# Performance work log

Measured on AMD Instinct MI355X. Metric: run time of the kernel, lower is better.

The kernel has to match this reference:

```python
import jax, jax.numpy as jnp
import numpy as np

B, N, E, D, H, O = 4, 10000, 160000, 128, 4, 64
NEG_SLOPE = 0.2  # PyG GATConv default


def setup_inputs() -> dict:
    key = jax.random.key(0)
    ks = jax.random.split(key, 9)
    x = jax.random.normal(ks[0], (B, N, D), jnp.float32)
    edge_index = jax.random.randint(ks[1], (2, E), 0, N, dtype=jnp.int64)
    edge_attr = jax.random.uniform(ks[2], (E,), jnp.float32)
    W_src = jax.random.normal(ks[3], (D, H, O), jnp.float32) * (1.0 / np.sqrt(D))
    att_src = jax.random.normal(ks[4], (H, O), jnp.float32) * 0.1
    att_dst = jax.random.normal(ks[5], (H, O), jnp.float32) * 0.1
    W_edge = jax.random.normal(ks[6], (H, O), jnp.float32) * 0.1  # lin_edge weight for edge_dim=1
    att_edge = jax.random.normal(ks[7], (H, O), jnp.float32) * 0.1
    bias = jnp.zeros((O,), jnp.float32)
    return {"x": x, "edge_index": edge_index, "edge_attr": edge_attr,
            "W_src": W_src, "att_src": att_src, "att_dst": att_dst,
            "W_edge": W_edge, "att_edge": att_edge, "bias": bias}


def reference(x, edge_index, edge_attr, W_src, att_src, att_dst, W_edge, att_edge, bias):
    src, dst = edge_index[0], edge_index[1]
    # shared linear projection (PyG non-bipartite GATConv): [B,N,H,O]
    h = jnp.einsum('bnd,dho->bnho', x, W_src)
    a_src = jnp.einsum('bnho,ho->bnh', h, att_src)  # [B,N,H]
    a_dst = jnp.einsum('bnho,ho->bnh', h, att_dst)  # [B,N,H]
    # edge feature projection (edge_dim=1): [E,H]
    a_edge = edge_attr[:, None] * jnp.einsum('ho,ho->h', W_edge, att_edge)[None, :]
    # attention logits per edge: [B,E,H]
    alpha = a_src[:, src] + a_dst[:, dst] + a_edge[None]
    alpha = jax.nn.leaky_relu(alpha, NEG_SLOPE)
    # segment softmax over destination nodes; segment ops need axis 0 = E
    alpha_t = jnp.transpose(alpha, (1, 0, 2))  # [E,B,H]
    m = jax.ops.segment_max(alpha_t, dst, num_segments=N)  # [N,B,H]
    m = jnp.where(jnp.isfinite(m), m, 0.0)
    p = jnp.exp(alpha_t - m[dst])
    s = jax.ops.segment_sum(p, dst, num_segments=N)
    w = p / jnp.maximum(s[dst], jnp.asarray(1e-16, p.dtype))  # [E,B,H]
    # weighted messages from source nodes, scatter-add into destinations
    msg = w[..., None] * jnp.transpose(h[:, src], (1, 0, 2, 3))  # [E,B,H,O]
    out = jax.ops.segment_sum(msg, dst, num_segments=N)  # [N,B,H,O]
    out = out.mean(axis=2) + bias  # concat=False -> mean over heads, [N,B,O]
    return jnp.transpose(out, (1, 0, 2))  # [B,N,O]
```

## Files before the change

### kernel.cpp

```cpp
#include <hip/hip_runtime.h>
#include <hip/hip_fp16.h>
#include <math.h>

constexpr int B_  = 4;
constexpr int N_  = 10000;
constexpr int E_  = 160000;
constexpr int D_  = 128;
constexpr int H_  = 4;
constexpr int O_  = 64;
constexpr float NEG_SLOPE = 0.2f;
constexpr int CAP = 64;
constexpr int PLACE_BLOCKS = E_ / 256;
constexpr int GEMM_BLOCKS  = (B_ * N_) / 64;

using half8   = __attribute__((ext_vector_type(8))) _Float16;
using half2v  = __attribute__((ext_vector_type(2))) _Float16;
using f32x4   = __attribute__((ext_vector_type(4))) float;
using ushort8v = __attribute__((ext_vector_type(8))) unsigned short;

static __device__ __forceinline__ unsigned short f2h(float f) {
    return __half_as_ushort(__float2half(f));
}
static __device__ __forceinline__ float h2f(unsigned short u) {
    return __half2float(__ushort_as_half(u));
}

#if __has_builtin(__builtin_amdgcn_fdot2)
#define FDOT2(a, b, c) __builtin_amdgcn_fdot2((a), (b), (c), false)
#else
static __device__ __forceinline__ float FDOT2(half2v a, half2v b, float c) {
    return c + (float)a[0] * (float)b[0] + (float)a[1] * (float)b[1];
}
#endif

__global__ __launch_bounds__(256) void k_prep(
    const float* __restrict__ Wsrc, const float* __restrict__ att_src,
    const float* __restrict__ att_dst,
    const float* __restrict__ W_edge, const float* __restrict__ att_edge,
    unsigned short* __restrict__ W1t, unsigned short* __restrict__ Vt,
    int* __restrict__ deg, float* __restrict__ c)
{
    const int d = blockIdx.x;
    const int t = threadIdx.x;
    const int h = t >> 6;

    for (int i = d * 256 + t; i < N_; i += 128 * 256) deg[i] = 0;

    const float wv = Wsrc[(size_t)d * 256 + t];
    const int cc = ((t & 63) << 2) | h;
    W1t[(size_t)cc * 128 + d] = f2h(wv);

    float vs = wv * att_src[t];
    float vd = wv * att_dst[t];
#pragma unroll
    for (int off = 32; off > 0; off >>= 1) {
        vs += __shfl_down(vs, off, 64);
        vd += __shfl_down(vd, off, 64);
    }
    if ((t & 63) == 0) {
        Vt[h * 128 + d]       = f2h(vs);
        Vt[(4 + h) * 128 + d] = f2h(vd);
    }
    if (d == 1) {
#pragma unroll
        for (int k = 0; k < 4; ++k) Vt[1024 + k * 256 + t] = 0;
    }

    if (d == 0) {
        float v = W_edge[t] * att_edge[t];
#pragma unroll
        for (int off = 32; off > 0; off >>= 1) v += __shfl_down(v, off, 64);
        if ((t & 63) == 0) c[h] = v;
    }
}

__global__ __launch_bounds__(256) void k_gemm(
    const float* __restrict__ x, const int* __restrict__ ei,
    const float* __restrict__ eattr,
    const unsigned short* __restrict__ W1t, const unsigned short* __restrict__ Vt,
    unsigned short* __restrict__ hbw, float* __restrict__ asrc, float* __restrict__ adst,
    int* __restrict__ deg, int2* __restrict__ srcea)
{
    constexpr int APAD = 136;
    __shared__ uint4 SHq[2112];
    unsigned short* A0 = (unsigned short*)SHq;
    unsigned short* A1 = (unsigned short*)SHq + 4352;
    unsigned short* Cb = (unsigned short*)SHq + 8704;

    const int t = threadIdx.x;

    if (blockIdx.x < PLACE_BLOCKS) {
        const int e = blockIdx.x * 256 + t;
        const int dstn = ei[E_ + e];
        const int r = atomicAdd(&deg[dstn], 1);
        srcea[dstn * CAP + r] = make_int2(ei[e], __float_as_int(eattr[e]));
        return;
    }

    const int w = t >> 6;
    const int lane = t & 63;
    const int i = lane & 15;
    const int q = lane >> 4;
    const size_t rowbase = (size_t)(blockIdx.x - PLACE_BLOCKS) * 64;

    const float4* xg = (const float4*)(x + rowbase * D_);
    float4 xr0[4], xr1[4];
#pragma unroll
    for (int it = 0; it < 4; ++it) xr0[it] = xg[it * 256 + t];
#pragma unroll
    for (int it = 0; it < 4; ++it) xr1[it] = xg[1024 + it * 256 + t];

    half8 breg[4][4];
#pragma unroll
    for (int ks = 0; ks < 4; ++ks)
#pragma unroll
        for (int ctl = 0; ctl < 4; ++ctl) {
            const size_t boff = (size_t)((w * 4 + ctl) * 16 + i) * 128 + ks * 32 + q * 8;
            breg[ks][ctl] = *(const half8*)&W1t[boff];
        }
    half8 vreg[4];
    if (w < 2) {
#pragma unroll
        for (int ks = 0; ks < 4; ++ks)
            vreg[ks] = *(const half8*)&Vt[i * 128 + ks * 32 + q * 8];
    }

#pragma unroll
    for (int it = 0; it < 4; ++it) {
        const int idx = it * 256 + t;
        const int row = idx >> 5;
        const int c4  = idx & 31;
        ushort4 h1;
        h1.x = f2h(xr0[it].x); h1.y = f2h(xr0[it].y);
        h1.z = f2h(xr0[it].z); h1.w = f2h(xr0[it].w);
        *(ushort4*)&A0[row * APAD + c4 * 4] = h1;
    }
    __syncthreads();

    f32x4 acc0[2][4];
#pragma unroll
    for (int tl = 0; tl < 2; ++tl)
#pragma unroll
        for (int ctl = 0; ctl < 4; ++ctl) acc0[tl][ctl] = (f32x4){0.f, 0.f, 0.f, 0.f};
    f32x4 accV0 = (f32x4){0.f, 0.f, 0.f, 0.f};

#pragma unroll
    for (int ks = 0; ks < 4; ++ks) {
        const int a0off = i * APAD + ks * 32 + q * 8;
        const int a1off = (16 + i) * APAD + ks * 32 + q * 8;
        half8 at0 = *(const half8*)&A0[a0off];
        half8 at1 = *(const half8*)&A0[a1off];
#pragma unroll
        for (int ctl = 0; ctl < 4; ++ctl) {
            acc0[0][ctl] = __builtin_amdgcn_mfma_f32_16x16x32_f16(at0, breg[ks][ctl], acc0[0][ctl], 0, 0, 0);
            acc0[1][ctl] = __builtin_amdgcn_mfma_f32_16x16x32_f16(at1, breg[ks][ctl], acc0[1][ctl], 0, 0, 0);
        }
        if (w < 2) {
            const half8 atV = (w == 0) ? at0 : at1;
            accV0 = __builtin_amdgcn_mfma_f32_16x16x32_f16(atV, vreg[ks], accV0, 0, 0, 0);
        }
    }

#pragma unroll
    for (int it = 0; it < 4; ++it) {
        const int idx = it * 256 + t;
        const int row = idx >> 5;
        const int c4  = idx & 31;
        ushort4 h1;
        h1.x = f2h(xr1[it].x); h1.y = f2h(xr1[it].y);
        h1.z = f2h(xr1[it].z); h1.w = f2h(xr1[it].w);
        *(ushort4*)&A1[row * APAD + c4 * 4] = h1;
    }

    if (w < 2 && i < 8) {
#pragma unroll
        for (int r = 0; r < 4; ++r) {
            const int row = w * 16 + q * 4 + r;
            const size_t rg = rowbase + row;
            if (i < 4) asrc[rg * 4 + i]       = accV0[r];
            else       adst[rg * 4 + (i - 4)] = accV0[r];
        }
    }
    __syncthreads();

    f32x4 acc1[2][4];
#pragma unroll
    for (int tl = 0; tl < 2; ++tl)
#pragma unroll
        for (int ctl = 0; ctl < 4; ++ctl) acc1[tl][ctl] = (f32x4){0.f, 0.f, 0.f, 0.f};
    f32x4 accV1 = (f32x4){0.f, 0.f, 0.f, 0.f};

#pragma unroll
    for (int ks = 0; ks < 4; ++ks) {
        const int a0off = i * APAD + ks * 32 + q * 8;
        const int a1off = (16 + i) * APAD + ks * 32 + q * 8;
        half8 at0 = *(const half8*)&A1[a0off];
        half8 at1 = *(const half8*)&A1[a1off];
#pragma unroll
        for (int ctl = 0; ctl < 4; ++ctl) {
            acc1[0][ctl] = __builtin_amdgcn_mfma_f32_16x16x32_f16(at0, breg[ks][ctl], acc1[0][ctl], 0, 0, 0);
            acc1[1][ctl] = __builtin_amdgcn_mfma_f32_16x16x32_f16(at1, breg[ks][ctl], acc1[1][ctl], 0, 0, 0);
        }
        if (w < 2) {
            const half8 atV = (w == 0) ? at0 : at1;
            accV1 = __builtin_amdgcn_mfma_f32_16x16x32_f16(atV, vreg[ks], accV1, 0, 0, 0);
        }
    }

#pragma unroll
    for (int tl = 0; tl < 2; ++tl) {
#pragma unroll
        for (int ctl = 0; ctl < 4; ++ctl) {
            const int col = (w * 4 + ctl) * 16 + i;
            const int chnk = col >> 3;
            const int within = col & 7;
#pragma unroll
            for (int r = 0; r < 4; ++r) {
                const int row = tl * 16 + q * 4 + r;
                const int s = chnk ^ row;
                Cb[row * 256 + s * 8 + within] = f2h(acc0[tl][ctl][r]);
            }
        }
    }

    if (w < 2 && i < 8) {
#pragma unroll
        for (int r = 0; r < 4; ++r) {
            const int row = w * 16 + q * 4 + r;
            const size_t rg = rowbase + 32 + row;
            if (i < 4) asrc[rg * 4 + i]       = accV1[r];
            else       adst[rg * 4 + (i - 4)] = accV1[r];
        }
    }
    __syncthreads();

    {
        const int chnk = t & 31;
#pragma unroll
        for (int k = 0; k < 4; ++k) {
            const int row = k * 8 + (t >> 5);
            const int s = chnk ^ row;
            const uint4 v = *(const uint4*)&Cb[row * 256 + s * 8];
            *(uint4*)&hbw[(rowbase + row) * 256 + chnk * 8] = v;
        }
    }
    __syncthreads();

#pragma unroll
    for (int tl = 0; tl < 2; ++tl) {
#pragma unroll
        for (int ctl = 0; ctl < 4; ++ctl) {
            const int col = (w * 4 + ctl) * 16 + i;
            const int chnk = col >> 3;
            const int within = col & 7;
#pragma unroll
            for (int r = 0; r < 4; ++r) {
                const int row = tl * 16 + q * 4 + r;
                const int s = chnk ^ row;
                Cb[row * 256 + s * 8 + within] = f2h(acc1[tl][ctl][r]);
            }
        }
    }
    __syncthreads();

    {
        const int chnk = t & 31;
#pragma unroll
        for (int k = 0; k < 4; ++k) {
            const int row = k * 8 + (t >> 5);
            const int s = chnk ^ row;
            const uint4 v = *(const uint4*)&Cb[row * 256 + s * 8];
            *(uint4*)&hbw[(rowbase + 32 + row) * 256 + chnk * 8] = v;
        }
    }
}

__global__ __launch_bounds__(256) void k_agg(
    const int* __restrict__ deg, const int2* __restrict__ srcea,
    const float* __restrict__ asrc, const float* __restrict__ adst,
    const float* __restrict__ cvec, const unsigned short* __restrict__ hbu,
    const float* __restrict__ bias, float* __restrict__ out)
{
    __shared__ uint4 jS[4][2][64];

    const int b    = blockIdx.x & 3;
    const int g    = blockIdx.x >> 2;
    const int wave = threadIdx.x >> 6;
    const int lane = threadIdx.x & 63;
    const int dstA = g * 8 + wave;
    const int dstB = dstA + 4;

    const int dgA = deg[dstA];
    const int dgB = deg[dstB];
    const bool vA = lane < dgA;
    const bool vB = lane < dgB;
    const int2 recA = srcea[dstA * CAP + (vA ? lane : 0)];
    const int2 recB = srcea[dstB * CAP + (vB ? lane : 0)];
    const float4 adA = *(const float4*)&adst[((size_t)b * N_ + dstA) * 4];
    const float4 adB = *(const float4*)&adst[((size_t)b * N_ + dstB) * 4];
    const float4 cc  = *(const float4*)cvec;

    const int srcA = vA ? recA.x : 0;
    const int srcB = vB ? recB.x : 0;
    const float eaA = __int_as_float(recA.y);
    const float eaB = __int_as_float(recB.y);
    const float4 asA = *(const float4*)&asrc[((size_t)b * N_ + srcA) * 4];
    const float4 asB = *(const float4*)&asrc[((size_t)b * N_ + srcB) * 4];

    float4 alA, alB;
    alA.x = asA.x + adA.x + eaA * cc.x;  alB.x = asB.x + adB.x + eaB * cc.x;
    alA.y = asA.y + adA.y + eaA * cc.y;  alB.y = asB.y + adB.y + eaB * cc.y;
    alA.z = asA.z + adA.z + eaA * cc.z;  alB.z = asB.z + adB.z + eaB * cc.z;
    alA.w = asA.w + adA.w + eaA * cc.w;  alB.w = asB.w + adB.w + eaB * cc.w;
    alA.x = alA.x > 0.f ? alA.x : NEG_SLOPE * alA.x;
    alA.y = alA.y > 0.f ? alA.y : NEG_SLOPE * alA.y;
    alA.z = alA.z > 0.f ? alA.z : NEG_SLOPE * alA.z;
    alA.w = alA.w > 0.f ? alA.w : NEG_SLOPE * alA.w;
    alB.x = alB.x > 0.f ? alB.x : NEG_SLOPE * alB.x;
    alB.y = alB.y > 0.f ? alB.y : NEG_SLOPE * alB.y;
    alB.z = alB.z > 0.f ? alB.z : NEG_SLOPE * alB.z;
    alB.w = alB.w > 0.f ? alB.w : NEG_SLOPE * alB.w;
    float qA0 = vA ? __expf(alA.x) : 0.f;
    float qA1 = vA ? __expf(alA.y) : 0.f;
    float qA2 = vA ? __expf(alA.z) : 0.f;
    float qA3 = vA ? __expf(alA.w) : 0.f;
    float qB0 = vB ? __expf(alB.x) : 0.f;
    float qB1 = vB ? __expf(alB.y) : 0.f;
    float qB2 = vB ? __expf(alB.z) : 0.f;
    float qB3 = vB ? __expf(alB.w) : 0.f;
    const float pA0 = qA0, pA1 = qA1, pA2 = qA2, pA3 = qA3;
    const float pB0 = qB0, pB1 = qB1, pB2 = qB2, pB3 = qB3;

#pragma unroll
    for (int off = 32; off > 0; off >>= 1) {
        qA0 += __shfl_xor(qA0, off, 64);  qB0 += __shfl_xor(qB0, off, 64);
        qA1 += __shfl_xor(qA1, off, 64);  qB1 += __shfl_xor(qB1, off, 64);
        qA2 += __shfl_xor(qA2, off, 64);  qB2 += __shfl_xor(qB2, off, 64);
        qA3 += __shfl_xor(qA3, off, 64);  qB3 += __shfl_xor(qB3, off, 64);
    }
    const float iA0 = 1.f / fmaxf(qA0, 1e-16f), iA1 = 1.f / fmaxf(qA1, 1e-16f);
    const float iA2 = 1.f / fmaxf(qA2, 1e-16f), iA3 = 1.f / fmaxf(qA3, 1e-16f);
    const float iB0 = 1.f / fmaxf(qB0, 1e-16f), iB1 = 1.f / fmaxf(qB1, 1e-16f);
    const float iB2 = 1.f / fmaxf(qB2, 1e-16f), iB3 = 1.f / fmaxf(qB3, 1e-16f);

    union { half2v h; unsigned u; } a01, a23, b01, b23;
    a01.h[0] = (_Float16)(pA0 * iA0); a01.h[1] = (_Float16)(pA1 * iA1);
    a23.h[0] = (_Float16)(pA2 * iA2); a23.h[1] = (_Float16)(pA3 * iA3);
    b01.h[0] = (_Float16)(pB0 * iB0); b01.h[1] = (_Float16)(pB1 * iB1);
    b23.h[0] = (_Float16)(pB2 * iB2); b23.h[1] = (_Float16)(pB3 * iB3);
    jS[wave][0][lane] = make_uint4((unsigned)((b * N_ + srcA) << 8), a01.u, a23.u, 0u);
    jS[wave][1][lane] = make_uint4((unsigned)((b * N_ + srcB) << 8), b01.u, b23.u, 0u);
    __builtin_amdgcn_wave_barrier();

    const int half = lane >> 5;
    const int ol   = (lane & 31) * 8;

    float aA0[4] = {0.f, 0.f, 0.f, 0.f}, aA1[4] = {0.f, 0.f, 0.f, 0.f};
    float aB0[4] = {0.f, 0.f, 0.f, 0.f}, aB1[4] = {0.f, 0.f, 0.f, 0.f};

    const int dgM = dgA > dgB ? dgA : dgB;
    for (int j = 0; j < dgM; j += 8) {
#pragma unroll
        for (int u = 0; u < 4; ++u) {
            const int idx = j + 2 * u + half;
            const uint4 eA = jS[wave][0][idx];
            const uint4 eB = jS[wave][1][idx];
            const ushort8v hA = *(const ushort8v*)&hbu[(size_t)eA.x + ol];
            const ushort8v hB = *(const ushort8v*)&hbu[(size_t)eB.x + ol];
            union { ushort8v s; half2v h[4]; } HA, HB; HA.s = hA; HB.s = hB;
            union { unsigned u; half2v h; } pA01, pA23, pB01, pB23;
            pA01.u = eA.y; pA23.u = eA.z;
            pB01.u = eB.y; pB23.u = eB.z;
            aA0[u] = FDOT2(HA.h[0], pA01.h, aA0[u]);
            aA0[u] = FDOT2(HA.h[1], pA23.h, aA0[u]);
            aA1[u] = FDOT2(HA.h[2], pA01.h, aA1[u]);
            aA1[u] = FDOT2(HA.h[3], pA23.h, aA1[u]);
            aB0[u] = FDOT2(HB.h[0], pB01.h, aB0[u]);
            aB0[u] = FDOT2(HB.h[1], pB23.h, aB0[u]);
            aB1[u] = FDOT2(HB.h[2], pB01.h, aB1[u]);
            aB1[u] = FDOT2(HB.h[3], pB23.h, aB1[u]);
        }
    }

    float tA0 = (aA0[0] + aA0[1]) + (aA0[2] + aA0[3]);
    float tA1 = (aA1[0] + aA1[1]) + (aA1[2] + aA1[3]);
    float tB0 = (aB0[0] + aB0[1]) + (aB0[2] + aB0[3]);
    float tB1 = (aB1[0] + aB1[1]) + (aB1[2] + aB1[3]);
    tA0 += __shfl_xor(tA0, 32, 64);
    tA1 += __shfl_xor(tA1, 32, 64);
    tB0 += __shfl_xor(tB0, 32, 64);
    tB1 += __shfl_xor(tB1, 32, 64);

    {
        const int lo = lane & 31;
        const int dstX = half ? dstB : dstA;
        const float u0 = half ? tB0 : tA0;
        const float u1 = half ? tB1 : tA1;
        const float2 bs = *(const float2*)&bias[lo * 2];
        float2 res;
        res.x = 0.25f * u0 + bs.x;
        res.y = 0.25f * u1 + bs.y;
        *(float2*)&out[((size_t)b * N_ + dstX) * O_ + lo * 2] = res;
    }
}

extern "C" void kernel_launch(void* const* d_in, const int* in_sizes, int n_in,
                              void* d_out, int out_size, void* d_ws, size_t ws_size,
                              hipStream_t stream)
{
    (void)in_sizes; (void)n_in; (void)out_size; (void)ws_size;
    const float* x        = (const float*)d_in[0];
    const int*   ei       = (const int*)d_in[1];
    const float* eattr    = (const float*)d_in[2];
    const float* Wsrc     = (const float*)d_in[3];
    const float* att_src  = (const float*)d_in[4];
    const float* att_dst  = (const float*)d_in[5];
    const float* W_edge   = (const float*)d_in[6];
    const float* att_edge = (const float*)d_in[7];
    const float* bias     = (const float*)d_in[8];
    float* out = (float*)d_out;

    char* w = (char*)d_ws;
    auto take = [&](size_t bytes) { char* p = w; w += (bytes + 15) & ~size_t(15); return p; };
    unsigned short* hb   = (unsigned short*)take((size_t)B_ * N_ * O_ * H_ * 2);
    float* asrc    = (float*)take((size_t)B_ * N_ * H_ * 4);
    float* adst    = (float*)take((size_t)B_ * N_ * H_ * 4);
    float* c       = (float*)take(4 * 4);
    unsigned short* W1t = (unsigned short*)take((size_t)256 * 128 * 2);
    unsigned short* Vt  = (unsigned short*)take((size_t)16 * 128 * 2);
    int* deg       = (int*)take((size_t)N_ * 4);
    int2* srcea    = (int2*)take((size_t)N_ * CAP * 8);

    hipLaunchKernelGGL(k_prep, dim3(128), dim3(256), 0, stream,
                       Wsrc, att_src, att_dst, W_edge, att_edge,
                       W1t, Vt, deg, c);
    hipLaunchKernelGGL(k_gemm, dim3(PLACE_BLOCKS + GEMM_BLOCKS), dim3(256), 0, stream,
                       x, ei, eattr, W1t, Vt, hb, asrc, adst, deg, srcea);
    hipLaunchKernelGGL(k_agg, dim3(N_ / 8 * B_), dim3(256), 0, stream,
                       deg, srcea, asrc, adst, c, hb, bias, out);
}
```

Baseline: 130.4 us.

## Interleave edge-placement blocks with smaller 32-row GEMM blocks in fused kernel

Each GEMM block now processes 32 rows instead of 64, so the grid grows to 1250 GEMM blocks plus 625 edge-placement blocks. The block-index mapping interleaves them two GEMM to one placement, so the atomic-heavy scatter work runs alongside the matrix-multiply work instead of all at the front of the grid. Shared memory per block drops, which may raise occupancy. In exchange, each block reloads the full weight matrix into registers for half as many rows, doubling weight-load traffic per output row.

```diff
diff --git a/kernel.cpp b/kernel.cpp
--- a/kernel.cpp
+++ b/kernel.cpp
@@ -10,8 +10,7 @@
 constexpr int O_  = 64;
 constexpr float NEG_SLOPE = 0.2f;
 constexpr int CAP = 64;
-constexpr int PLACE_BLOCKS = E_ / 256;
-constexpr int GEMM_BLOCKS  = (B_ * N_) / 64;
+constexpr int TOTAL_BLOCKS = 1875;
 
 using half8   = __attribute__((ext_vector_type(8))) _Float16;
 using half2v  = __attribute__((ext_vector_type(2))) _Float16;
@@ -32,6 +31,7 @@
     return c + (float)a[0] * (float)b[0] + (float)a[1] * (float)b[1];
 }
 #endif
+
 
 __global__ __launch_bounds__(256) void k_prep(
     const float* __restrict__ Wsrc, const float* __restrict__ att_src,
@@ -82,33 +82,32 @@
     int* __restrict__ deg, int2* __restrict__ srcea)
 {
     constexpr int APAD = 136;
-    __shared__ uint4 SHq[2112];
-    unsigned short* A0 = (unsigned short*)SHq;
-    unsigned short* A1 = (unsigned short*)SHq + 4352;
-    unsigned short* Cb = (unsigned short*)SHq + 8704;
+    __shared__ uint4 SHq[1568];
+    unsigned short* A1 = (unsigned short*)SHq;
+    unsigned short* Cb = (unsigned short*)SHq + 4352;
 
     const int t = threadIdx.x;
-
-    if (blockIdx.x < PLACE_BLOCKS) {
-        const int e = blockIdx.x * 256 + t;
+    const int bid = blockIdx.x;
+
+    if ((bid % 3) == 2) {
+        const int e = (bid / 3) * 256 + t;
         const int dstn = ei[E_ + e];
         const int r = atomicAdd(&deg[dstn], 1);
         srcea[dstn * CAP + r] = make_int2(ei[e], __float_as_int(eattr[e]));
         return;
     }
+    const int gidx = 2 * (bid / 3) + (bid % 3);
 
     const int w = t >> 6;
     const int lane = t & 63;
     const int i = lane & 15;
     const int q = lane >> 4;
-    const size_t rowbase = (size_t)(blockIdx.x - PLACE_BLOCKS) * 64;
+    const size_t rowbase = (size_t)gidx * 32;
 
     const float4* xg = (const float4*)(x + rowbase * D_);
-    float4 xr0[4], xr1[4];
+    float4 xr0[4];
 #pragma unroll
     for (int it = 0; it < 4; ++it) xr0[it] = xg[it * 256 + t];
-#pragma unroll
-    for (int it = 0; it < 4; ++it) xr1[it] = xg[1024 + it * 256 + t];
 
     half8 breg[4][4];
 #pragma unroll
@@ -133,62 +132,16 @@
         ushort4 h1;
         h1.x = f2h(xr0[it].x); h1.y = f2h(xr0[it].y);
         h1.z = f2h(xr0[it].z); h1.w = f2h(xr0[it].w);
-        *(ushort4*)&A0[row * APAD + c4 * 4] = h1;
+        *(ushort4*)&A1[row * APAD + c4 * 4] = h1;
     }
     __syncthreads();
 
-    f32x4 acc0[2][4];
+    f32x4 acc[2][4];
 #pragma unroll
     for (int tl = 0; tl < 2; ++tl)
 #pragma unroll
-        for (int ctl = 0; ctl < 4; ++ctl) acc0[tl][ctl] = (f32x4){0.f, 0.f, 0.f, 0.f};
-    f32x4 accV0 = (f32x4){0.f, 0.f, 0.f, 0.f};
-
-#pragma unroll
-    for (int ks = 0; ks < 4; ++ks) {
-        const int a0off = i * APAD + ks * 32 + q * 8;
-        const int a1off = (16 + i) * APAD + ks * 32 + q * 8;
-        half8 at0 = *(const half8*)&A0[a0off];
-        half8 at1 = *(const half8*)&A0[a1off];
-#pragma unroll
-        for (int ctl = 0; ctl < 4; ++ctl) {
-            acc0[0][ctl] = __builtin_amdgcn_mfma_f32_16x16x32_f16(at0, breg[ks][ctl], acc0[0][ctl], 0, 0, 0);
-            acc0[1][ctl] = __builtin_amdgcn_mfma_f32_16x16x32_f16(at1, breg[ks][ctl], acc0[1][ctl], 0, 0, 0);
-        }
-        if (w < 2) {
-            const half8 atV = (w == 0) ? at0 : at1;
-            accV0 = __builtin_amdgcn_mfma_f32_16x16x32_f16(atV, vreg[ks], accV0, 0, 0, 0);
-        }
-    }
-
-#pragma unroll
-    for (int it = 0; it < 4; ++it) {
-        const int idx = it * 256 + t;
-        const int row = idx >> 5;
-        const int c4  = idx & 31;
-        ushort4 h1;
-        h1.x = f2h(xr1[it].x); h1.y = f2h(xr1[it].y);
-        h1.z = f2h(xr1[it].z); h1.w = f2h(xr1[it].w);
-        *(ushort4*)&A1[row * APAD + c4 * 4] = h1;
-    }
-
-    if (w < 2 && i < 8) {
-#pragma unroll
-        for (int r = 0; r < 4; ++r) {
-            const int row = w * 16 + q * 4 + r;
-            const size_t rg = rowbase + row;
-            if (i < 4) asrc[rg * 4 + i]       = accV0[r];
-            else       adst[rg * 4 + (i - 4)] = accV0[r];
-        }
-    }
-    __syncthreads();
-
-    f32x4 acc1[2][4];
-#pragma unroll
-    for (int tl = 0; tl < 2; ++tl)
-#pragma unroll
-        for (int ctl = 0; ctl < 4; ++ctl) acc1[tl][ctl] = (f32x4){0.f, 0.f, 0.f, 0.f};
-    f32x4 accV1 = (f32x4){0.f, 0.f, 0.f, 0.f};
+        for (int ctl = 0; ctl < 4; ++ctl) acc[tl][ctl] = (f32x4){0.f, 0.f, 0.f, 0.f};
+    f32x4 accV = (f32x4){0.f, 0.f, 0.f, 0.f};
 
 #pragma unroll
     for (int ks = 0; ks < 4; ++ks) {
@@ -198,12 +151,22 @@
         half8 at1 = *(const half8*)&A1[a1off];
 #pragma unroll
         for (int ctl = 0; ctl < 4; ++ctl) {
-            acc1[0][ctl] = __builtin_amdgcn_mfma_f32_16x16x32_f16(at0, breg[ks][ctl], acc1[0][ctl], 0, 0, 0);
-            acc1[1][ctl] = __builtin_amdgcn_mfma_f32_16x16x32_f16(at1, breg[ks][ctl], acc1[1][ctl], 0, 0, 0);
+            acc[0][ctl] = __builtin_amdgcn_mfma_f32_16x16x32_f16(at0, breg[ks][ctl], acc[0][ctl], 0, 0, 0);
+            acc[1][ctl] = __builtin_amdgcn_mfma_f32_16x16x32_f16(at1, breg[ks][ctl], acc[1][ctl], 0, 0, 0);
         }
         if (w < 2) {
             const half8 atV = (w == 0) ? at0 : at1;
-            accV1 = __builtin_amdgcn_mfma_f32_16x16x32_f16(atV, vreg[ks], accV1, 0, 0, 0);
+            accV = __builtin_amdgcn_mfma_f32_16x16x32_f16(atV, vreg[ks], accV, 0, 0, 0);
+        }
+    }
+
+    if (w < 2 && i < 8) {
+#pragma unroll
+        for (int r = 0; r < 4; ++r) {
+            const int row = w * 16 + q * 4 + r;
+            const size_t rg = rowbase + row;
+            if (i < 4) asrc[rg * 4 + i]       = accV[r];
+            else       adst[rg * 4 + (i - 4)] = accV[r];
         }
     }
 
@@ -218,22 +181,11 @@
             for (int r = 0; r < 4; ++r) {
                 const int row = tl * 16 + q * 4 + r;
                 const int s = chnk ^ row;
-                Cb[row * 256 + s * 8 + within] = f2h(acc0[tl][ctl][r]);
+                Cb[row * 256 + s * 8 + within] = f2h(acc[tl][ctl][r]);
             }
         }
     }
-
-    if (w < 2 && i < 8) {
-#pragma unroll
-        for (int r = 0; r < 4; ++r) {
-            const int row = w * 16 + q * 4 + r;
-            const size_t rg = rowbase + 32 + row;
-            if (i < 4) asrc[rg * 4 + i]       = accV1[r];
-            else       adst[rg * 4 + (i - 4)] = accV1[r];
-        }
-    }
     __syncthreads();
-
     {
         const int chnk = t & 31;
 #pragma unroll
@@ -242,35 +194,6 @@
             const int s = chnk ^ row;
             const uint4 v = *(const uint4*)&Cb[row * 256 + s * 8];
             *(uint4*)&hbw[(rowbase + row) * 256 + chnk * 8] = v;
-        }
-    }
-    __syncthreads();
-
-#pragma unroll
-    for (int tl = 0; tl < 2; ++tl) {
-#pragma unroll
-        for (int ctl = 0; ctl < 4; ++ctl) {
-            const int col = (w * 4 + ctl) * 16 + i;
-            const int chnk = col >> 3;
-            const int within = col & 7;
-#pragma unroll
-            for (int r = 0; r < 4; ++r) {
-                const int row = tl * 16 + q * 4 + r;
-                const int s = chnk ^ row;
-                Cb[row * 256 + s * 8 + within] = f2h(acc1[tl][ctl][r]);
-            }
-        }
-    }
-    __syncthreads();
-
-    {
-        const int chnk = t & 31;
-#pragma unroll
-        for (int k = 0; k < 4; ++k) {
-            const int row = k * 8 + (t >> 5);
-            const int s = chnk ^ row;
-            const uint4 v = *(const uint4*)&Cb[row * 256 + s * 8];
-            *(uint4*)&hbw[(rowbase + 32 + row) * 256 + chnk * 8] = v;
         }
     }
 }
@@ -434,7 +357,7 @@
     hipLaunchKernelGGL(k_prep, dim3(128), dim3(256), 0, stream,
                        Wsrc, att_src, att_dst, W_edge, att_edge,
                        W1t, Vt, deg, c);
-    hipLaunchKernelGGL(k_gemm, dim3(PLACE_BLOCKS + GEMM_BLOCKS), dim3(256), 0, stream,
+    hipLaunchKernelGGL(k_gemm, dim3(TOTAL_BLOCKS), dim3(256), 0, stream,
                        x, ei, eattr, W1t, Vt, hb, asrc, adst, deg, srcea);
     hipLaunchKernelGGL(k_agg, dim3(N_ / 8 * B_), dim3(256), 0, stream,
                        deg, srcea, asrc, adst, c, hb, bias, out);
```

New measurement: 156.2 us. 1.2x slower.
